# Kernel optimization log

Measured on AMD Instinct MI355X. Metric: run time of the kernel, lower is better.

## Reference

```python
import jax, jax.numpy as jnp
import numpy as np

B, CIN, H, W = 2, 128, 64, 64
CHNN = 32
SC = 100.0


def conv1x1(x, w, b=None):
    # x: (b,c,h,w), w: (o,c)
    y = jnp.einsum('bchw,oc->bohw', x, w)
    return y if b is None else y + b[None, :, None, None]


def depthwise5x5_replicate(x, w, b):
    # x: (b,c,h,w), w: (c,1,5,5), replicate (edge) padding of 2
    xp = jnp.pad(x, ((0, 0), (0, 0), (2, 2), (2, 2)), mode='edge')
    y = jax.lax.conv_general_dilated(xp, w, (1, 1), 'VALID',
                                     feature_group_count=x.shape[1])
    return y + b[None, :, None, None]


def grid_sample_bilinear(img, grid):
    # img: (b,C,Hs,Ws); grid: (b,h,w,2) with (x,y) in [-1,1]; align_corners=True
    b, C, Hs, Ws = img.shape
    x = (grid[..., 0] + 1.0) * 0.5 * (Ws - 1)
    y = (grid[..., 1] + 1.0) * 0.5 * (Hs - 1)
    x0 = jnp.floor(x); y0 = jnp.floor(y)
    wx1 = x - x0; wx0 = 1.0 - wx1
    wy1 = y - y0; wy0 = 1.0 - wy1
    x0i = jnp.clip(x0, 0, Ws - 1).astype(jnp.int32)
    x1i = jnp.clip(x0 + 1, 0, Ws - 1).astype(jnp.int32)
    y0i = jnp.clip(y0, 0, Hs - 1).astype(jnp.int32)
    y1i = jnp.clip(y0 + 1, 0, Hs - 1).astype(jnp.int32)
    imgf = img.reshape(b, C, Hs * Ws)

    def gather(idx):  # idx: (b,h,w) int32 -> (b,C,h,w)
        idxf = idx.reshape(b, -1)
        out = jax.vmap(lambda im, ix: im[:, ix])(imgf, idxf)
        return out.reshape(b, C, idx.shape[1], idx.shape[2])

    v00 = gather(y0i * Ws + x0i)
    v01 = gather(y0i * Ws + x1i)
    v10 = gather(y1i * Ws + x0i)
    v11 = gather(y1i * Ws + x1i)
    return (v00 * (wy0 * wx0)[:, None] + v01 * (wy0 * wx1)[:, None]
            + v10 * (wy1 * wx0)[:, None] + v11 * (wy1 * wx1)[:, None])


def setup_inputs() -> dict:
    key = jax.random.key(0)
    ks = jax.random.split(key, 8)
    return {
        'feat': jax.random.normal(ks[0], (B, CIN, H, W), jnp.float32),
        'gauss': jax.random.uniform(ks[1], (B, H, W, H, W), jnp.float32),
        'W_in': jax.random.normal(ks[2], (CHNN, 1), jnp.float32) * 0.1,
        'b_in': jnp.zeros((CHNN,), jnp.float32),
        'W_dw': jax.random.normal(ks[3], (CHNN, 1, 5, 5), jnp.float32) * 0.1,
        'b_dw': jnp.zeros((CHNN,), jnp.float32),
        'W_ofs': jax.random.normal(ks[4], (2, CHNN), jnp.float32) * 0.1,
        'W_a': jax.random.normal(ks[5], (1, CHNN), jnp.float32) * 0.1,
        'b_a': jnp.zeros((1,), jnp.float32),
        'lam': jnp.full((1,), 0.1, jnp.float32),
    }


def reference(feat, gauss, W_in, b_in, W_dw, b_dw, W_ofs, W_a, b_a, lam):
    b, _, h, w = feat.shape
    fm = feat.mean(1, keepdims=True)                       # (b,1,h,w)
    feat_in = conv1x1(fm, W_in, b_in)                      # (b,chnn,h,w)
    z = jax.nn.relu(depthwise5x5_replicate(feat_in, W_dw, b_dw))
    ofs = jnp.tanh(conv1x1(z, W_ofs))                      # (b,2,h,w)
    scale = jnp.array([1.0 / h, 1.0 / w], dtype=feat.dtype).reshape(1, 2, 1, 1)
    ofs = jnp.transpose(ofs * scale, (0, 2, 3, 1))         # (b,h,w,2) as (y,x)
    yy = (jnp.linspace(0.5, h - 0.5, h, dtype=feat.dtype) / h) * 2.0 - 1.0
    xx = (jnp.linspace(0.5, w - 0.5, w, dtype=feat.dtype) / w) * 2.0 - 1.0
    ref = jnp.stack(jnp.meshgrid(yy, xx, indexing='ij'), -1)  # (h,w,2)
    pos = jnp.clip(SC * ofs + ref[None], -1.0, 1.0)
    grid = pos[..., ::-1]                                  # (x,y) order
    # gauss (b,u,v,h,w) -> rearrange to (b,h,w,u,v) -> flatten (h,w) as channels
    g = jnp.transpose(gauss, (0, 3, 4, 1, 2)).reshape(b, h * w, h, w)
    gd = grid_sample_bilinear(g, grid).reshape(b, h, w, h, w)
    feat_a = conv1x1(feat_in, W_a, b_a)                    # (b,1,h,w)
    ga = 1.0 + lam[0] * feat_a                             # (b,1,h,w)
    return gd * ga[:, :, None, :, :]
```

## Files before the change

### kernel.cpp

```cpp
#include <hip/hip_runtime.h>
#include <math.h>

#define HW 64
#define NB 2
#define NCIN 128
#define NCH 32

typedef float f32x4 __attribute__((ext_vector_type(4)));


__global__ __launch_bounds__(256) void k_mean(const float* __restrict__ feat,
                                              float* __restrict__ fm) {
    int bh = blockIdx.x;
    int w  = threadIdx.x & 63;
    int cg = threadIdx.x >> 6;
    int b = bh >> 6, h = bh & 63;
    const float* base = feat + ((size_t)(b * NCIN) * 64 + h) * 64 + w;
    float s = 0.f;
    #pragma unroll
    for (int c = 0; c < 32; ++c)
        s += base[(size_t)(cg * 32 + c) * 4096];
    __shared__ float red[4][64];
    red[cg][w] = s;
    __syncthreads();
    if (cg == 0) {
        float tot = red[0][w] + red[1][w] + red[2][w] + red[3][w];
        fm[bh * 64 + w] = tot * (1.f / 128.f);
    }
}

__global__ __launch_bounds__(256) void k_params(
    const float* __restrict__ fm,
    const float* __restrict__ W_in, const float* __restrict__ b_in,
    const float* __restrict__ W_dw, const float* __restrict__ b_dw,
    const float* __restrict__ W_ofs, const float* __restrict__ W_a,
    const float* __restrict__ b_a, const float* __restrict__ lam,
    int4* __restrict__ offs, float4* __restrict__ wts)
{
    __shared__ float WD[NCH * 25];
    __shared__ float Wi[NCH], Bi[NCH], Bd[NCH], Wo0[NCH], Wo1[NCH], Wa_s[NCH];
    int t = threadIdx.x;
    for (int k = t; k < NCH * 25; k += 256) WD[k] = W_dw[k];
    if (t < NCH) {
        Wi[t]  = W_in[t];  Bi[t]  = b_in[t]; Bd[t] = b_dw[t];
        Wo0[t] = W_ofs[t]; Wo1[t] = W_ofs[NCH + t];
        Wa_s[t] = W_a[t];
    }
    __syncthreads();

    int p = blockIdx.x * 256 + t;
    int b = p >> 12;
    int i = (p >> 6) & 63;
    int j = p & 63;

    float patch[25];
    #pragma unroll
    for (int dy = 0; dy < 5; ++dy) {
        int ry = i + dy - 2; ry = ry < 0 ? 0 : (ry > 63 ? 63 : ry);
        #pragma unroll
        for (int dx = 0; dx < 5; ++dx) {
            int rx = j + dx - 2; rx = rx < 0 ? 0 : (rx > 63 ? 63 : rx);
            patch[dy * 5 + dx] = fm[(b * 64 + ry) * 64 + rx];
        }
    }
    float fmc = patch[12];

    float a0 = 0.f, a1 = 0.f, kA = 0.f, kB = 0.f;
    for (int c = 0; c < NCH; ++c) {
        float s = 0.f, sw = 0.f;
        #pragma unroll
        for (int q = 0; q < 25; ++q) {
            float wv = WD[c * 25 + q];
            s  += patch[q] * wv;
            sw += wv;
        }
        float pre = Wi[c] * s + Bi[c] * sw + Bd[c];
        float zc = pre > 0.f ? pre : 0.f;
        a0 += zc * Wo0[c];
        a1 += zc * Wo1[c];
        kA += Wi[c] * Wa_s[c];
        kB += Bi[c] * Wa_s[c];
    }
    float ga = 1.f + lam[0] * (fmc * kA + kB + b_a[0]);

    float yy = (i + 0.5f) * (1.f / 32.f) - 1.f;
    float xx = (j + 0.5f) * (1.f / 32.f) - 1.f;
    float pos0 = fminf(fmaxf((100.f / 64.f) * tanhf(a0) + yy, -1.f), 1.f);
    float pos1 = fminf(fmaxf((100.f / 64.f) * tanhf(a1) + xx, -1.f), 1.f);
    float y = (pos0 + 1.f) * 0.5f * 63.f;
    float x = (pos1 + 1.f) * 0.5f * 63.f;
    float y0 = floorf(y), x0 = floorf(x);
    float wy1 = y - y0, wx1 = x - x0;
    float wy0 = 1.f - wy1, wx0 = 1.f - wx1;
    int y0i = (int)y0; y0i = y0i < 0 ? 0 : (y0i > 63 ? 63 : y0i);
    int x0i = (int)x0; x0i = x0i < 0 ? 0 : (x0i > 63 ? 63 : x0i);
    int y1i = y0i + 1 > 63 ? 63 : y0i + 1;
    int x1i = x0i + 1 > 63 ? 63 : x0i + 1;

    int basep = b * 16777216;
    offs[p] = make_int4(basep + (y0i * 64 + x0i) * 4096,
                        basep + (y0i * 64 + x1i) * 4096,
                        basep + (y1i * 64 + x0i) * 4096,
                        basep + (y1i * 64 + x1i) * 4096);
    wts[p] = make_float4(wy0 * wx0 * ga, wy0 * wx1 * ga,
                         wy1 * wx0 * ga, wy1 * wx1 * ga);
}

__global__ __launch_bounds__(256) void k_sample(
    const float* __restrict__ gauss,
    const int4* __restrict__ offs, const float4* __restrict__ wts,
    float* __restrict__ out)
{
    __shared__ float lds[32 * 128];
    int bid = blockIdx.x;
    int swz = (bid & 7) * 1024 + (bid >> 3);
    int bi  = swz >> 6;
    int ct  = (swz >> 1) & 31;
    int jh  = swz & 1;
    int b = bi >> 6, i = bi & 63;
    int c0 = ct * 128;
    int t  = threadIdx.x;
    int pbase = bi * 64 + jh * 32;

    int h  = t & 31;
    int js = t >> 5;

    #pragma unroll
    for (int r = 0; r < 4; ++r) {
        int j = r * 8 + js;
        int4  off = offs[pbase + j];
        float4 wt = wts[pbase + j];
        f32x4 A = *((const f32x4*)(gauss + off.x + c0) + h);
        f32x4 B = *((const f32x4*)(gauss + off.y + c0) + h);
        f32x4 C = *((const f32x4*)(gauss + off.z + c0) + h);
        f32x4 D = *((const f32x4*)(gauss + off.w + c0) + h);
        f32x4 res = wt.x * A + wt.y * B + wt.z * C + wt.w * D;
        *(f32x4*)&lds[j * 128 + 4 * (h ^ (j & 15))] = res;
    }
    __syncthreads();

    size_t obase = (size_t)b * 16777216 + (size_t)c0 * 4096
                 + (size_t)i * 64 + jh * 32;
    int j2 = t & 31;
    int cg = t >> 5;
    int f  = j2 & 15;
    #pragma unroll
    for (int m = 0; m < 4; ++m) {
        int q = m * 8 + cg;
        f32x4 v = *(const f32x4*)&lds[j2 * 128 + 4 * (q ^ f)];
        float* po = out + obase + (size_t)(q * 4) * 4096 + j2;
        __builtin_nontemporal_store(v.x, po);
        __builtin_nontemporal_store(v.y, po + 4096);
        __builtin_nontemporal_store(v.z, po + 8192);
        __builtin_nontemporal_store(v.w, po + 12288);
    }
}

extern "C" void kernel_launch(void* const* d_in, const int* in_sizes, int n_in,
                              void* d_out, int out_size, void* d_ws, size_t ws_size,
                              hipStream_t stream) {
    const float* feat  = (const float*)d_in[0];
    const float* gauss = (const float*)d_in[1];
    const float* W_in  = (const float*)d_in[2];
    const float* b_in  = (const float*)d_in[3];
    const float* W_dw  = (const float*)d_in[4];
    const float* b_dw  = (const float*)d_in[5];
    const float* W_ofs = (const float*)d_in[6];
    const float* W_a   = (const float*)d_in[7];
    const float* b_a   = (const float*)d_in[8];
    const float* lam   = (const float*)d_in[9];
    float* out = (float*)d_out;

    float* fm   = (float*)d_ws;
    int4*  offs = (int4*)((char*)d_ws + 32768);
    float4* wts = (float4*)((char*)d_ws + 32768 + 131072);

    k_mean  <<<NB * HW, 256, 0, stream>>>(feat, fm);
    k_params<<<32, 256, 0, stream>>>(fm, W_in, b_in, W_dw, b_dw,
                                     W_ofs, W_a, b_a, lam, offs, wts);
    k_sample<<<NB * HW * 64, 256, 0, stream>>>(gauss, offs, wts, out);
}
```

Measured before the change: 63.11 us.

## Stage bounding box of sampled source cells in LDS to dedupe gathers

Each sample block now works out the bounding box of all source cells its 32 output pixels need, using a wave shuffle reduction over packed indices. If the box holds at most 80 cells, it loads each cell's 128-channel slice into LDS once and does the bilinear blend from LDS, so neighbouring pixels no longer fetch the same gauss rows repeatedly. Otherwise it falls back to direct global gathers. Indices are packed into one int per pixel. The cost is a larger LDS footprint (40KB), which may reduce occupancy, plus extra integer div/mod work in the staging loop.

```diff
diff --git a/kernel.cpp b/kernel.cpp
--- a/kernel.cpp
+++ b/kernel.cpp
@@ -35,7 +35,7 @@
     const float* __restrict__ W_dw, const float* __restrict__ b_dw,
     const float* __restrict__ W_ofs, const float* __restrict__ W_a,
     const float* __restrict__ b_a, const float* __restrict__ lam,
-    int4* __restrict__ offs, float4* __restrict__ wts)
+    int* __restrict__ pk, float4* __restrict__ wts)
 {
     __shared__ float WD[NCH * 25];
     __shared__ float Wi[NCH], Bi[NCH], Bd[NCH], Wo0[NCH], Wo1[NCH], Wa_s[NCH];
@@ -97,21 +97,17 @@
     int y1i = y0i + 1 > 63 ? 63 : y0i + 1;
     int x1i = x0i + 1 > 63 ? 63 : x0i + 1;
 
-    int basep = b * 16777216;
-    offs[p] = make_int4(basep + (y0i * 64 + x0i) * 4096,
-                        basep + (y0i * 64 + x1i) * 4096,
-                        basep + (y1i * 64 + x0i) * 4096,
-                        basep + (y1i * 64 + x1i) * 4096);
+    pk[p] = y0i | (y1i << 6) | (x0i << 12) | (x1i << 18);
     wts[p] = make_float4(wy0 * wx0 * ga, wy0 * wx1 * ga,
                          wy1 * wx0 * ga, wy1 * wx1 * ga);
 }
 
 __global__ __launch_bounds__(256) void k_sample(
     const float* __restrict__ gauss,
-    const int4* __restrict__ offs, const float4* __restrict__ wts,
+    const int* __restrict__ pk, const float4* __restrict__ wts,
     float* __restrict__ out)
 {
-    __shared__ float lds[32 * 128];
+    __shared__ float lds[80 * 128];
     int bid = blockIdx.x;
     int swz = (bid & 7) * 1024 + (bid >> 3);
     int bi  = swz >> 6;
@@ -122,37 +118,76 @@
     int t  = threadIdx.x;
     int pbase = bi * 64 + jh * 32;
 
-    int h  = t & 31;
-    int js = t >> 5;
-
+    int myj = t & 31;
+    int pv  = pk[pbase + myj];
+    int py0 = pv & 63, py1 = (pv >> 6) & 63;
+    int px0 = (pv >> 12) & 63, px1 = (pv >> 18) & 63;
+    int ymin = min(py0, py1), ymax = max(py0, py1);
+    int xmin = min(px0, px1), xmax = max(px0, px1);
     #pragma unroll
-    for (int r = 0; r < 4; ++r) {
-        int j = r * 8 + js;
-        int4  off = offs[pbase + j];
-        float4 wt = wts[pbase + j];
-        f32x4 A = *((const f32x4*)(gauss + off.x + c0) + h);
-        f32x4 B = *((const f32x4*)(gauss + off.y + c0) + h);
-        f32x4 C = *((const f32x4*)(gauss + off.z + c0) + h);
-        f32x4 D = *((const f32x4*)(gauss + off.w + c0) + h);
-        f32x4 res = wt.x * A + wt.y * B + wt.z * C + wt.w * D;
-        *(f32x4*)&lds[j * 128 + 4 * (h ^ (j & 15))] = res;
-    }
-    __syncthreads();
-
+    for (int d = 1; d <= 16; d <<= 1) {
+        ymin = min(ymin, __shfl_xor(ymin, d));
+        ymax = max(ymax, __shfl_xor(ymax, d));
+        xmin = min(xmin, __shfl_xor(xmin, d));
+        xmax = max(xmax, __shfl_xor(xmax, d));
+    }
+    int W = xmax - xmin + 1;
+    int H = ymax - ymin + 1;
+    int ncell = W * H;
+
+    const float* gbase = gauss + (size_t)b * 16777216 + c0;
+    float4 wt = wts[pbase + myj];
     size_t obase = (size_t)b * 16777216 + (size_t)c0 * 4096
-                 + (size_t)i * 64 + jh * 32;
-    int j2 = t & 31;
+                 + (size_t)i * 64 + jh * 32 + myj;
     int cg = t >> 5;
-    int f  = j2 & 15;
-    #pragma unroll
-    for (int m = 0; m < 4; ++m) {
-        int q = m * 8 + cg;
-        f32x4 v = *(const f32x4*)&lds[j2 * 128 + 4 * (q ^ f)];
-        float* po = out + obase + (size_t)(q * 4) * 4096 + j2;
-        __builtin_nontemporal_store(v.x, po);
-        __builtin_nontemporal_store(v.y, po + 4096);
-        __builtin_nontemporal_store(v.z, po + 8192);
-        __builtin_nontemporal_store(v.w, po + 12288);
+
+    if (ncell <= 80) {
+        int nquad = ncell << 5;
+        for (int kq = t; kq < nquad; kq += 256) {
+            int cell = kq >> 5, m = kq & 31;
+            int cy = ymin + cell / W, cx = xmin + cell % W;
+            f32x4 v = *(const f32x4*)(gbase + (size_t)(cy * 64 + cx) * 4096 + 4 * m);
+            *(f32x4*)&lds[cell * 128 + 4 * ((m + cell) & 31)] = v;
+        }
+        __syncthreads();
+
+        int ca = (py0 - ymin) * W + (px0 - xmin);
+        int cb = (py0 - ymin) * W + (px1 - xmin);
+        int cc = (py1 - ymin) * W + (px0 - xmin);
+        int cd = (py1 - ymin) * W + (px1 - xmin);
+        #pragma unroll
+        for (int m = 0; m < 4; ++m) {
+            int q = m * 8 + cg;
+            f32x4 A = *(const f32x4*)&lds[ca * 128 + 4 * ((q + ca) & 31)];
+            f32x4 B = *(const f32x4*)&lds[cb * 128 + 4 * ((q + cb) & 31)];
+            f32x4 C = *(const f32x4*)&lds[cc * 128 + 4 * ((q + cc) & 31)];
+            f32x4 D = *(const f32x4*)&lds[cd * 128 + 4 * ((q + cd) & 31)];
+            f32x4 res = wt.x * A + wt.y * B + wt.z * C + wt.w * D;
+            float* po = out + obase + (size_t)(q * 4) * 4096;
+            __builtin_nontemporal_store(res.x, po);
+            __builtin_nontemporal_store(res.y, po + 4096);
+            __builtin_nontemporal_store(res.z, po + 8192);
+            __builtin_nontemporal_store(res.w, po + 12288);
+        }
+    } else {
+        size_t fa = (size_t)(py0 * 64 + px0) * 4096;
+        size_t fb = (size_t)(py0 * 64 + px1) * 4096;
+        size_t fc = (size_t)(py1 * 64 + px0) * 4096;
+        size_t fd = (size_t)(py1 * 64 + px1) * 4096;
+        #pragma unroll
+        for (int m = 0; m < 4; ++m) {
+            int q = m * 8 + cg;
+            f32x4 A = *(const f32x4*)(gbase + fa + 4 * q);
+            f32x4 B = *(const f32x4*)(gbase + fb + 4 * q);
+            f32x4 C = *(const f32x4*)(gbase + fc + 4 * q);
+            f32x4 D = *(const f32x4*)(gbase + fd + 4 * q);
+            f32x4 res = wt.x * A + wt.y * B + wt.z * C + wt.w * D;
+            float* po = out + obase + (size_t)(q * 4) * 4096;
+            __builtin_nontemporal_store(res.x, po);
+            __builtin_nontemporal_store(res.y, po + 4096);
+            __builtin_nontemporal_store(res.z, po + 8192);
+            __builtin_nontemporal_store(res.w, po + 12288);
+        }
     }
 }
 
@@ -171,12 +206,12 @@
     const float* lam   = (const float*)d_in[9];
     float* out = (float*)d_out;
 
-    float* fm   = (float*)d_ws;
-    int4*  offs = (int4*)((char*)d_ws + 32768);
-    float4* wts = (float4*)((char*)d_ws + 32768 + 131072);
+    float*  fm  = (float*)d_ws;
+    int*    pk  = (int*)((char*)d_ws + 32768);
+    float4* wts = (float4*)((char*)d_ws + 65536);
 
     k_mean  <<<NB * HW, 256, 0, stream>>>(feat, fm);
     k_params<<<32, 256, 0, stream>>>(fm, W_in, b_in, W_dw, b_dw,
-                                     W_ofs, W_a, b_a, lam, offs, wts);
-    k_sample<<<NB * HW * 64, 256, 0, stream>>>(gauss, offs, wts, out);
-}
+                                     W_ofs, W_a, b_a, lam, pk, wts);
+    k_sample<<<NB * HW * 64, 256, 0, stream>>>(gauss, pk, wts, out);
+}
```

Result: slower. 83.87 us (+32.9%).
